# Optimization experiments

Hardware: AMD Instinct MI355X
Metric: run time of the kernel (lower is better)

## Reference

```python
import jax, jax.numpy as jnp
import numpy as np

BATCH, NUM_POINTS, DIM, NUM_PROJS = 32, 4096, 3, 256


def _sobol_2d(n):
    """Unscrambled 2D Sobol sequence (Joe-Kuo direction numbers), first point = 0,
    matching torch.quasirandom.SobolEngine(dimension=2, scramble=False).draw(n)."""
    bits = 32
    V = np.zeros((2, bits), dtype=np.uint64)
    for j in range(bits):
        V[0, j] = np.uint64(1) << np.uint64(bits - 1 - j)  # van der Corput
    m = [1]
    for i in range(1, bits):
        m.append((2 * m[i - 1]) ^ m[i - 1])  # s=1, a=0 recurrence -> 1,3,5,15,17,...
    for j in range(bits):
        V[1, j] = np.uint64(m[j]) << np.uint64(bits - 1 - j)
    x = np.zeros(2, dtype=np.uint64)
    pts = np.zeros((n, 2), dtype=np.float64)
    for i in range(1, n):
        c, v = 0, i - 1
        while v & 1:
            v >>= 1
            c += 1
        x ^= V[:, c]
        pts[i] = x / float(2 ** bits)
    return pts


def setup_inputs() -> dict:
    key = jax.random.key(0)
    kx, ky, kr = jax.random.split(key, 3)
    x = jax.random.normal(kx, (BATCH, NUM_POINTS, DIM), dtype=jnp.float32)
    y = jax.random.normal(ky, (BATCH, NUM_POINTS, DIM), dtype=jnp.float32)

    # Sobol points -> uniform directions on S^2 (as in the torch module)
    net = _sobol_2d(NUM_PROJS)
    alpha, tau = net[:, 0], net[:, 1]
    r = 2.0 * np.sqrt(np.clip(tau - tau ** 2, 0.0, None))
    theta = np.stack([r * np.cos(2 * np.pi * alpha),
                      r * np.sin(2 * np.pi * alpha),
                      1.0 - 2.0 * tau], axis=1).astype(np.float32)  # [P,3]

    # Per-sample random rotation: Q of QR(randn(3,3)), batched
    g = np.asarray(jax.random.normal(kr, (BATCH, DIM, DIM), dtype=jnp.float32))
    rotations = np.linalg.qr(g.astype(np.float64))[0].astype(np.float32)  # [B,3,3]

    return {"x": x, "y": y, "theta": jnp.asarray(theta), "rotations": jnp.asarray(rotations)}


def reference(x, y, theta, rotations):
    # rotated projections: [B, P, 3]
    proj = jnp.einsum('pd,bde->bpe', theta, rotations)
    # project point clouds: [B, P, N]
    xp = jnp.einsum('bnd,bpd->bpn', x, proj)
    yp = jnp.einsum('bnd,bpd->bpn', y, proj)
    # sorted 1D Wasserstein-2 per projection
    d = jnp.sort(xp, axis=-1) - jnp.sort(yp, axis=-1)
    per_proj = jnp.sum(d * d, axis=-1)              # [B, P]  (|.|^2, degree=2)
    dist = jnp.sqrt(jnp.mean(per_proj, axis=1))     # [B]
    return jnp.mean(dist)
```

## Files before the change

### kernel.cpp

```cpp
#include <hip/hip_runtime.h>
#include <math.h>

#define NPTS 4096
#define BLK 128
#define V 64
#define NPROJ 256
#define NBATCH 32


__device__ __forceinline__ void cmpex_asc(float& a, float& b) {
    const float lo = fminf(a, b), hi = fmaxf(a, b);
    a = lo; b = hi;
}

template<int JB, int JL>
__device__ __forceinline__ void stages(float* v) {
#pragma unroll
    for (int r = 0; r < V; ++r)
        if ((r & JB) == 0) cmpex_asc(v[r], v[r | JB]);
    if constexpr (JB > JL) stages<(JB >> 1), JL>(v);
}

template<int MASK>
__device__ __forceinline__ void rev_inreg(float* v) {
    constexpr int S = (MASK + 1) >> 1;
#pragma unroll
    for (int r = 0; r < V; ++r) {
        if ((r & S) == 0) {
            const float a = v[r], b = v[r ^ MASK];
            v[r] = fminf(a, b);
            v[r ^ MASK] = fmaxf(a, b);
        }
    }
}

template<int XM>
__device__ __forceinline__ void rev_shfl(float* v, bool hi) {
#pragma unroll
    for (int r = 0; r < 32; ++r) {
        const float pa = __shfl_xor(v[63 - r], XM, 64);
        const float pb = __shfl_xor(v[r], XM, 64);
        v[r]      = hi ? fmaxf(v[r], pa)      : fminf(v[r], pa);
        v[63 - r] = hi ? fmaxf(v[63 - r], pb) : fminf(v[63 - r], pb);
    }
}
template<int XM>
__device__ __forceinline__ void stage_shfl(float* v, bool hi) {
#pragma unroll
    for (int r = 0; r < V; ++r) {
        const float q = __shfl_xor(v[r], XM, 64);
        v[r] = hi ? fmaxf(v[r], q) : fminf(v[r], q);
    }
}

__device__ __forceinline__ void write_AB(float* s, const float* v, int sAB, int t15) {
    float4* s4 = (float4*)s;
#pragma unroll
    for (int c = 0; c < 16; ++c)
        s4[sAB | (c << 4) | (t15 ^ c)] =
            make_float4(v[4*c], v[4*c+1], v[4*c+2], v[4*c+3]);
}
__device__ __forceinline__ void write_own(float* s, const float* v, int t, int t15) {
    float4* s4 = (float4*)s;
#pragma unroll
    for (int c = 0; c < 16; ++c)
        s4[(t << 4) | (c ^ t15)] =
            make_float4(v[4*c], v[4*c+1], v[4*c+2], v[4*c+3]);
}
__device__ __forceinline__ void read_own(const float* s, float* v, int t, int t15) {
    const float4* s4 = (const float4*)s;
#pragma unroll
    for (int c = 0; c < 16; ++c) {
        const float4 f = s4[(t << 4) | (c ^ t15)];
        v[4*c] = f.x; v[4*c+1] = f.y; v[4*c+2] = f.z; v[4*c+3] = f.w;
    }
}
template<int PM, int CM, int KB>
__device__ __forceinline__ void read_rev_B(const float* s, float* v, int t, int t15, bool thi) {
    const float4* s4 = (const float4*)s;
    const int pt = t ^ PM, pt15 = t15 ^ (PM & 15);
#pragma unroll
    for (int c = 0; c < 16; ++c) {
        const float4 o = s4[(t << 4) | (c ^ t15)];
        const float4 q = s4[(pt << 4) | ((c ^ CM) ^ pt15)];
        const bool mx = KB ? ((c & KB) != 0) : thi;
        v[4*c+0] = mx ? fmaxf(o.x, q.w) : fminf(o.x, q.w);
        v[4*c+1] = mx ? fmaxf(o.y, q.z) : fminf(o.y, q.z);
        v[4*c+2] = mx ? fmaxf(o.z, q.y) : fminf(o.z, q.y);
        v[4*c+3] = mx ? fmaxf(o.w, q.x) : fminf(o.w, q.x);
    }
}
__device__ __forceinline__ void write_AC(float* s, const float* v, int t15, int qAC) {
    float4* s4 = (float4*)s;
#pragma unroll
    for (int c = 0; c < 16; ++c)
        s4[(t15 << 6) | ((c >> 2) << 4) | (qAC ^ (c & 3))] =
            make_float4(v[4*c], v[4*c+1], v[4*c+2], v[4*c+3]);
}
__device__ __forceinline__ void read_rev_C(const float* s, float* v, int t, int th) {
    const float4* s4 = (const float4*)s;
    const int pt = t ^ 63, pth = th ^ 15;
#pragma unroll
    for (int c = 0; c < 16; ++c) {
        const float4 o = s4[(t << 4) | (c ^ th)];
        const float4 q = s4[(pt << 4) | ((c ^ 15) ^ pth)];
        const bool mx = (c & 8) != 0;
        v[4*c+0] = mx ? fmaxf(o.x, q.w) : fminf(o.x, q.w);
        v[4*c+1] = mx ? fmaxf(o.y, q.z) : fminf(o.y, q.z);
        v[4*c+2] = mx ? fmaxf(o.z, q.y) : fminf(o.z, q.y);
        v[4*c+3] = mx ? fmaxf(o.w, q.x) : fminf(o.w, q.x);
    }
}
__device__ __forceinline__ void write_CB(float* s, const float* v, int sCB, int qCB) {
    float4* s4 = (float4*)s;
#pragma unroll
    for (int c = 0; c < 16; ++c)
        s4[((c >> 2) << 8) | sCB | ((c & 3) << 4) | (qCB ^ (c & 3))] =
            make_float4(v[4*c], v[4*c+1], v[4*c+2], v[4*c+3]);
}

__device__ __forceinline__ void sort4096(float* v, float* buf, int t) {
    const int t15 = t & 15;
    const int sAB = (t >> 4) << 8;
    const int qAC = ((t >> 4) << 2) ^ t15;
    const int th  = (t >> 2) & 15;
    const int sCB = (t & 3) << 6;
    const int qCB = (t >> 2) ^ ((t & 3) << 2);
    const bool hi1  = (t & 1) != 0;
    const bool hi2  = (t & 2) != 0;
    const bool hi16 = (t & 16) != 0;

    rev_inreg<1>(v);
    rev_inreg<3>(v);  stages<1, 1>(v);
    rev_inreg<7>(v);  stages<2, 1>(v);
    rev_inreg<15>(v); stages<4, 1>(v);
    rev_inreg<31>(v); stages<8, 1>(v);
    rev_inreg<63>(v); stages<16, 1>(v);

    rev_shfl<1>(v, hi1);
    stages<32, 1>(v);

    rev_shfl<3>(v, hi2);
    stage_shfl<2>(v, hi2);
    stage_shfl<1>(v, hi1);
    stages<32, 1>(v);

    write_AB(buf, v, sAB, t15);
    read_rev_B<15, 7, 4>(buf, v, t, t15, false);
    stages<8, 4>(v);
    write_AB(buf, v, sAB, t15);
    read_own(buf, v, t, t15);
    stages<32, 1>(v);

    write_AB(buf, v, sAB, t15);
    read_rev_B<15, 15, 8>(buf, v, t, t15, false);
    stages<16, 4>(v);
    write_AB(buf, v, sAB, t15);
    read_own(buf, v, t, t15);
    stages<32, 1>(v);

    write_AB(buf, v, sAB, t15);
    read_rev_B<31, 15, 0>(buf, v, t, t15, hi16);
    stages<32, 4>(v);
    write_AB(buf, v, sAB, t15);
    read_own(buf, v, t, t15);
    stages<32, 1>(v);

    write_AC(buf, v, t15, qAC);
    read_rev_C(buf, v, t, th);
    stages<16, 16>(v);
    write_CB(buf, v, sCB, qCB);
    read_own(buf, v, t, t15);
    stages<32, 4>(v);
    write_AB(buf, v, sAB, t15);
    read_own(buf, v, t, t15);
    stages<32, 1>(v);
}

__device__ __forceinline__ void load_project(const float* base, float* v,
                                             float p0, float p1, float p2) {
    const float4* b4 = (const float4*)base;
#pragma unroll
    for (int g = 0; g < 16; ++g) {
        float4 a = b4[g * 3 + 0], c = b4[g * 3 + 1], d = b4[g * 3 + 2];
        v[4*g+0] = a.x * p0 + a.y * p1 + a.z * p2;
        v[4*g+1] = a.w * p0 + c.x * p1 + c.y * p2;
        v[4*g+2] = c.z * p0 + c.w * p1 + d.x * p2;
        v[4*g+3] = d.y * p0 + d.z * p1 + d.w * p2;
    }
}

__global__ __launch_bounds__(BLK, 2) void swd_kernel(
    const float* __restrict__ x, const float* __restrict__ y,
    const float* __restrict__ theta, const float* __restrict__ rot,
    float* __restrict__ per_batch) {
    __shared__ float buf2[2][NPTS];

    const int t = threadIdx.x & 63;
    const int wave = threadIdx.x >> 6;
    const int p = blockIdx.x;
    const int b = blockIdx.y;

    const float t0 = theta[p * 3 + 0], t1 = theta[p * 3 + 1], t2 = theta[p * 3 + 2];
    const float* R = rot + b * 9;
    const float p0 = t0 * R[0] + t1 * R[3] + t2 * R[6];
    const float p1 = t0 * R[1] + t1 * R[4] + t2 * R[7];
    const float p2 = t0 * R[2] + t1 * R[5] + t2 * R[8];

    float* buf = buf2[wave];
    const float* src = wave ? y : x;

    float v[V];
    load_project(src + (size_t)b * NPTS * 3 + (size_t)t * V * 3, v, p0, p1, p2);
    sort4096(v, buf, t);

    const int t15 = t & 15;
    if (wave == 1) write_own(buf2[1], v, t, t15);
    __syncthreads();

    if (wave == 0) {
        float w[V];
        read_own(buf2[1], w, t, t15);
        float s = 0.0f;
#pragma unroll
        for (int r = 0; r < V; ++r) {
            const float d = v[r] - w[r];
            s += d * d;
        }
        for (int off = 32; off > 0; off >>= 1) s += __shfl_down(s, off, 64);
        if (t == 0) atomicAdd(&per_batch[b], s);
    }
}

__global__ void finalize_kernel(const float* __restrict__ per_batch, float* __restrict__ out) {
    const int t = threadIdx.x;
    float v = (t < NBATCH) ? sqrtf(per_batch[t] * (1.0f / (float)NPROJ)) : 0.0f;
    for (int off = 32; off > 0; off >>= 1) v += __shfl_down(v, off, 64);
    if (t == 0) out[0] = v * (1.0f / (float)NBATCH);
}

extern "C" void kernel_launch(void* const* d_in, const int* in_sizes, int n_in,
                              void* d_out, int out_size, void* d_ws, size_t ws_size,
                              hipStream_t stream) {
    const float* x = (const float*)d_in[0];
    const float* y = (const float*)d_in[1];
    const float* theta = (const float*)d_in[2];
    const float* rot = (const float*)d_in[3];
    float* per_batch = (float*)d_ws;
    float* out = (float*)d_out;

    hipMemsetAsync(per_batch, 0, NBATCH * sizeof(float), stream);

    dim3 grid(NPROJ, NBATCH);
    swd_kernel<<<grid, BLK, 0, stream>>>(x, y, theta, rot, per_batch);

    finalize_kernel<<<1, 64, 0, stream>>>(per_batch, out);
}
```

Measured before the change: 372.7 us.

## Share LDS buffer between x/y sort waves with staggered transpose phases

The x and y sorting waves of a projection now share one LDS buffer and alternate transpose phases separated by block barriers. While one wave does its shared-memory transpose, the other runs its register compare-exchange stages. Blocks now process two projections with 256 threads, and launch bounds allow more blocks per CU. The aim is to halve LDS per projection and raise occupancy, at the cost of many extra barriers and possible register pressure.

Result: slower. 661.2 us (+77.4%).

```diff
diff --git a/kernel.cpp b/kernel.cpp
--- a/kernel.cpp
+++ b/kernel.cpp
@@ -2,7 +2,7 @@
 #include <math.h>
 
 #define NPTS 4096
-#define BLK 128
+#define BLK 256
 #define V 64
 #define NPROJ 256
 #define NBATCH 32
@@ -119,7 +119,43 @@
             make_float4(v[4*c], v[4*c+1], v[4*c+2], v[4*c+3]);
 }
 
-__device__ __forceinline__ void sort4096(float* v, float* buf, int t) {
+__device__ __forceinline__ void load_project(const float* base, float* v,
+                                             float p0, float p1, float p2) {
+    const float4* b4 = (const float4*)base;
+#pragma unroll
+    for (int g = 0; g < 16; ++g) {
+        float4 a = b4[g * 3 + 0], c = b4[g * 3 + 1], d = b4[g * 3 + 2];
+        v[4*g+0] = a.x * p0 + a.y * p1 + a.z * p2;
+        v[4*g+1] = a.w * p0 + c.x * p1 + c.y * p2;
+        v[4*g+2] = c.z * p0 + c.w * p1 + d.x * p2;
+        v[4*g+3] = d.y * p0 + d.z * p1 + d.w * p2;
+    }
+}
+
+__global__ __launch_bounds__(BLK, 4) void swd_kernel(
+    const float* __restrict__ x, const float* __restrict__ y,
+    const float* __restrict__ theta, const float* __restrict__ rot,
+    float* __restrict__ per_batch) {
+    __shared__ float buf2[2][NPTS];
+
+    const int t = threadIdx.x & 63;
+    const int w = (threadIdx.x >> 6) & 1;
+    const int pairId = threadIdx.x >> 7;
+    const int p = blockIdx.x * 2 + pairId;
+    const int b = blockIdx.y;
+
+    const float t0 = theta[p * 3 + 0], t1 = theta[p * 3 + 1], t2 = theta[p * 3 + 2];
+    const float* R = rot + b * 9;
+    const float p0 = t0 * R[0] + t1 * R[3] + t2 * R[6];
+    const float p1 = t0 * R[1] + t1 * R[4] + t2 * R[7];
+    const float p2 = t0 * R[2] + t1 * R[5] + t2 * R[8];
+
+    float* buf = buf2[pairId];
+    const float* src = w ? y : x;
+
+    float v[V];
+    load_project(src + (size_t)b * NPTS * 3 + (size_t)t * V * 3, v, p0, p1, p2);
+
     const int t15 = t & 15;
     const int sAB = (t >> 4) << 8;
     const int qAC = ((t >> 4) << 2) ^ t15;
@@ -136,95 +172,48 @@
     rev_inreg<15>(v); stages<4, 1>(v);
     rev_inreg<31>(v); stages<8, 1>(v);
     rev_inreg<63>(v); stages<16, 1>(v);
-
     rev_shfl<1>(v, hi1);
     stages<32, 1>(v);
-
     rev_shfl<3>(v, hi2);
     stage_shfl<2>(v, hi2);
     stage_shfl<1>(v, hi1);
     stages<32, 1>(v);
 
-    write_AB(buf, v, sAB, t15);
-    read_rev_B<15, 7, 4>(buf, v, t, t15, false);
-    stages<8, 4>(v);
-    write_AB(buf, v, sAB, t15);
-    read_own(buf, v, t, t15);
-    stages<32, 1>(v);
-
-    write_AB(buf, v, sAB, t15);
-    read_rev_B<15, 15, 8>(buf, v, t, t15, false);
-    stages<16, 4>(v);
-    write_AB(buf, v, sAB, t15);
-    read_own(buf, v, t, t15);
-    stages<32, 1>(v);
-
-    write_AB(buf, v, sAB, t15);
-    read_rev_B<31, 15, 0>(buf, v, t, t15, hi16);
-    stages<32, 4>(v);
-    write_AB(buf, v, sAB, t15);
-    read_own(buf, v, t, t15);
-    stages<32, 1>(v);
-
-    write_AC(buf, v, t15, qAC);
-    read_rev_C(buf, v, t, th);
-    stages<16, 16>(v);
-    write_CB(buf, v, sCB, qCB);
-    read_own(buf, v, t, t15);
-    stages<32, 4>(v);
-    write_AB(buf, v, sAB, t15);
-    read_own(buf, v, t, t15);
-    stages<32, 1>(v);
-}
-
-__device__ __forceinline__ void load_project(const float* base, float* v,
-                                             float p0, float p1, float p2) {
-    const float4* b4 = (const float4*)base;
-#pragma unroll
-    for (int g = 0; g < 16; ++g) {
-        float4 a = b4[g * 3 + 0], c = b4[g * 3 + 1], d = b4[g * 3 + 2];
-        v[4*g+0] = a.x * p0 + a.y * p1 + a.z * p2;
-        v[4*g+1] = a.w * p0 + c.x * p1 + c.y * p2;
-        v[4*g+2] = c.z * p0 + c.w * p1 + d.x * p2;
-        v[4*g+3] = d.y * p0 + d.z * p1 + d.w * p2;
-    }
-}
-
-__global__ __launch_bounds__(BLK, 2) void swd_kernel(
-    const float* __restrict__ x, const float* __restrict__ y,
-    const float* __restrict__ theta, const float* __restrict__ rot,
-    float* __restrict__ per_batch) {
-    __shared__ float buf2[2][NPTS];
-
-    const int t = threadIdx.x & 63;
-    const int wave = threadIdx.x >> 6;
-    const int p = blockIdx.x;
-    const int b = blockIdx.y;
-
-    const float t0 = theta[p * 3 + 0], t1 = theta[p * 3 + 1], t2 = theta[p * 3 + 2];
-    const float* R = rot + b * 9;
-    const float p0 = t0 * R[0] + t1 * R[3] + t2 * R[6];
-    const float p1 = t0 * R[1] + t1 * R[4] + t2 * R[7];
-    const float p2 = t0 * R[2] + t1 * R[5] + t2 * R[8];
-
-    float* buf = buf2[wave];
-    const float* src = wave ? y : x;
-
-    float v[V];
-    load_project(src + (size_t)b * NPTS * 3 + (size_t)t * V * 3, v, p0, p1, p2);
-    sort4096(v, buf, t);
-
-    const int t15 = t & 15;
-    if (wave == 1) write_own(buf2[1], v, t, t15);
-    __syncthreads();
-
-    if (wave == 0) {
-        float w[V];
-        read_own(buf2[1], w, t, t15);
+#define T_REV512  { write_AB(buf, v, sAB, t15); read_rev_B<15, 7, 4>(buf, v, t, t15, false); }
+#define T_REV1024 { write_AB(buf, v, sAB, t15); read_rev_B<15, 15, 8>(buf, v, t, t15, false); }
+#define T_REV2048 { write_AB(buf, v, sAB, t15); read_rev_B<31, 15, 0>(buf, v, t, t15, hi16); }
+#define T_OWN     { write_AB(buf, v, sAB, t15); read_own(buf, v, t, t15); }
+#define T_AC4096  { write_AC(buf, v, t15, qAC); read_rev_C(buf, v, t, th); }
+#define T_CB4096  { write_CB(buf, v, sCB, qCB); read_own(buf, v, t, t15); }
+#define SYNC __syncthreads();
+
+    SYNC if (!w) T_REV512
+    SYNC if (w)  T_REV512  else { stages<8, 4>(v); }
+    SYNC if (!w) T_OWN     else { stages<8, 4>(v); }
+    SYNC if (w)  T_OWN     else { stages<32, 1>(v); }
+    SYNC if (!w) T_REV1024 else { stages<32, 1>(v); }
+    SYNC if (w)  T_REV1024 else { stages<16, 4>(v); }
+    SYNC if (!w) T_OWN     else { stages<16, 4>(v); }
+    SYNC if (w)  T_OWN     else { stages<32, 1>(v); }
+    SYNC if (!w) T_REV2048 else { stages<32, 1>(v); }
+    SYNC if (w)  T_REV2048 else { stages<32, 4>(v); }
+    SYNC if (!w) T_OWN     else { stages<32, 4>(v); }
+    SYNC if (w)  T_OWN     else { stages<32, 1>(v); }
+    SYNC if (!w) T_AC4096  else { stages<32, 1>(v); }
+    SYNC if (w)  T_AC4096  else { stages<16, 16>(v); }
+    SYNC if (!w) T_CB4096  else { stages<16, 16>(v); }
+    SYNC if (w)  T_CB4096  else { stages<32, 4>(v); }
+    SYNC if (!w) T_OWN     else { stages<32, 4>(v); }
+    SYNC if (w)  T_OWN     else { stages<32, 1>(v); }
+    SYNC if (w)  { stages<32, 1>(v); write_own(buf, v, t, t15); }
+    SYNC
+    if (!w) {
+        float yv[V];
+        read_own(buf, yv, t, t15);
         float s = 0.0f;
 #pragma unroll
         for (int r = 0; r < V; ++r) {
-            const float d = v[r] - w[r];
+            const float d = v[r] - yv[r];
             s += d * d;
         }
         for (int off = 32; off > 0; off >>= 1) s += __shfl_down(s, off, 64);
@@ -251,7 +240,7 @@
 
     hipMemsetAsync(per_batch, 0, NBATCH * sizeof(float), stream);
 
-    dim3 grid(NPROJ, NBATCH);
+    dim3 grid(NPROJ / 2, NBATCH);
     swd_kernel<<<grid, BLK, 0, stream>>>(x, y, theta, rot, per_batch);
 
     finalize_kernel<<<1, 64, 0, stream>>>(per_batch, out);
```
